# Performance work log

Measured on AMD Instinct MI355X. Metric: run time of the kernel, lower is better.

## Reference

```python
import jax, jax.numpy as jnp
import numpy as np

HEADS = 4
DIM_HEAD = 128

def setup_inputs() -> dict:
    key = jax.random.key(0)
    k1, k2, k3, k4 = jax.random.split(key, 4)
    scale = DIM_HEAD ** -0.5
    return {
        "fmap": jax.random.normal(k1, (16, 512, 32, 32), dtype=jnp.float32),
        "w_qkv": jax.random.normal(k2, (1536, 512), dtype=jnp.float32) * 0.02,
        "height": jax.random.normal(k3, (32, DIM_HEAD), dtype=jnp.float32) * scale,
        "width": jax.random.normal(k4, (32, DIM_HEAD), dtype=jnp.float32) * scale,
    }

def reference(fmap, w_qkv, height, width):
    b, c, h, w = fmap.shape
    scale = DIM_HEAD ** -0.5
    # 1x1 conv == channel GEMM: (b, 3*heads*dim_head, h, w)
    qkv = jnp.einsum('bchw,oc->bohw', fmap, w_qkv)
    # split into q,k,v and reshape to (b, heads, seq, dim_head)
    qkv = qkv.reshape(b, 3, HEADS, DIM_HEAD, h * w)
    q, k, v = (jnp.transpose(qkv[:, i], (0, 1, 3, 2)) for i in range(3))
    # content logits
    sim = jnp.einsum('bhid,bhjd->bhij', q, k) * scale
    # absolute positional bias: emb[(x,y)] = height[x] + width[y]
    emb = (height[:, None, :] + width[None, :, :]).reshape(h * w, DIM_HEAD)
    sim = sim + jnp.einsum('bhid,jd->bhij', q, emb) * scale
    attn = jax.nn.softmax(sim, axis=-1)
    out = jnp.einsum('bhij,bhjd->bhid', attn, v)  # (b, heads, seq, d)
    out = jnp.transpose(out, (0, 1, 3, 2)).reshape(b, HEADS * DIM_HEAD, h, w)
    return out
```

## Files before the change

kernel.cpp:

```cpp
#include <hip/hip_runtime.h>
#include <math.h>

#define HEADS 4
#define DIMH  128
#define NB    16
#define CIN   512
#define SEQ   1024
#define OTOT  1536
#define KQ    (CIN / 8)

typedef __attribute__((ext_vector_type(8)))  short bf16x8;
typedef __attribute__((ext_vector_type(4)))  short bf16x4;
typedef __attribute__((ext_vector_type(4)))  float f32x4;
typedef __attribute__((ext_vector_type(16))) float f32x16;

#define MFMA16(a,b,c) __builtin_amdgcn_mfma_f32_16x16x32_bf16(a,b,c,0,0,0)
#define MFMA32(a,b,c) __builtin_amdgcn_mfma_f32_32x32x16_bf16(a,b,c,0,0,0)

__device__ __forceinline__ short f2bf(float f) {
    unsigned u = __builtin_bit_cast(unsigned, f);
    u = (u + 0x7FFFu + ((u >> 16) & 1u)) >> 16;
    return (short)u;
}
__device__ __forceinline__ unsigned pk2(float lo, float hi) {
    return __builtin_amdgcn_perm(__builtin_bit_cast(unsigned, hi),
                                 __builtin_bit_cast(unsigned, lo), 0x07060302u);
}
union PF8 { unsigned u[4]; bf16x8 v; };

__global__ __launch_bounds__(256) void convert_all(const float* __restrict__ F,
                                                   const float* __restrict__ W,
                                                   short* __restrict__ FT2,
                                                   short* __restrict__ Wb2) {
    const int kq = blockIdx.y;
    if (blockIdx.z == NB) {
        const int o = blockIdx.x * 256 + threadIdx.x;
        float4 v0 = *(const float4*)&W[(size_t)o * CIN + kq * 8];
        float4 v1 = *(const float4*)&W[(size_t)o * CIN + kq * 8 + 4];
        bf16x8 pk = { f2bf(v0.x), f2bf(v0.y), f2bf(v0.z), f2bf(v0.w),
                      f2bf(v1.x), f2bf(v1.y), f2bf(v1.z), f2bf(v1.w) };
        *(bf16x8*)&Wb2[((size_t)kq * OTOT + o) * 8] = pk;
        return;
    }
    if (blockIdx.x >= 4) return;
    const int s = blockIdx.x * 256 + threadIdx.x;
    const int b = blockIdx.z;
    const float* src = F + ((size_t)b * CIN + kq * 8) * SEQ + s;
    float v[8];
    #pragma unroll
    for (int i = 0; i < 8; ++i) v[i] = src[(size_t)i * SEQ];
    bf16x8 pk = { f2bf(v[0]), f2bf(v[1]), f2bf(v[2]), f2bf(v[3]),
                  f2bf(v[4]), f2bf(v[5]), f2bf(v[6]), f2bf(v[7]) };
    *(bf16x8*)&FT2[(((size_t)b * KQ + kq) * SEQ + s) * 8] = pk;
}

__global__ __launch_bounds__(256, 3) void qkv_gemm(
    const short* __restrict__ Wb2, const short* __restrict__ FT2,
    const float* __restrict__ height, const float* __restrict__ width,
    short* __restrict__ Qo, short* __restrict__ Kfo, short* __restrict__ Vfo)
{
    const int L  = blockIdx.x;
    const int x8 = L & 7, m = L >> 3;
    const int g  = x8 + 8 * (m / 12);
    const int oy = m % 12;
    const int b  = g >> 3, sx = g & 7;
    const int o0 = oy * 128, s0 = sx * 128;

    const int t = threadIdx.x, l = t & 63, w = t >> 6;
    const int quad = l >> 4, ln = l & 15;
    const int wrow = (w >> 1) * 64, wcol = (w & 1) * 64;

    const short* Ap = Wb2 + (((size_t)quad * OTOT) + (o0 + wrow + ln)) * 8;
    const short* Bp = FT2 + ((((size_t)b * KQ + quad) * SEQ) + (s0 + wcol + ln)) * 8;

    f32x4 acc[4][4] = {};
    bf16x8 a0[4], b0[4], a1[4], b1[4];

#define GLOADF(ks, af, bfr) { \
    const short* ga = Ap + (size_t)(ks) * 4 * OTOT * 8; \
    const short* gb = Bp + (size_t)(ks) * 4 * SEQ * 8; \
    _Pragma("unroll") for (int i = 0; i < 4; ++i) af[i]  = *(const bf16x8*)(ga + (size_t)i * 16 * 8); \
    _Pragma("unroll") for (int j = 0; j < 4; ++j) bfr[j] = *(const bf16x8*)(gb + (size_t)j * 16 * 8); }
#define COMP(af, bfr) { \
    _Pragma("unroll") for (int i = 0; i < 4; ++i) \
        _Pragma("unroll") for (int j = 0; j < 4; ++j) \
            acc[i][j] = MFMA16(af[i], bfr[j], acc[i][j]); }

    GLOADF(0, a0, b0);
    GLOADF(1, a1, b1);
    for (int ks = 0; ks < 16; ks += 2) {
        COMP(a0, b0);
        if (ks + 2 < 16) GLOADF(ks + 2, a0, b0);
        COMP(a1, b1);
        if (ks + 3 < 16) GLOADF(ks + 3, a1, b1);
    }

    const int sec = o0 >> 9;
    const int h   = (o0 >> 7) & 3;
    const size_t bh = (size_t)b * HEADS + h;

    if (sec == 0) {
        const float qs = 0.08838834764831845f * 1.4426950408889634f;
        #pragma unroll
        for (int ti = 0; ti < 4; ++ti) {
            int d = wrow + ti * 16 + quad * 4;
            #pragma unroll
            for (int tj = 0; tj < 4; ++tj) {
                int s = s0 + wcol + tj * 16 + ln;
                f32x4 a = acc[ti][tj];
                bf16x4 pk4 = { f2bf(a[0]*qs), f2bf(a[1]*qs), f2bf(a[2]*qs), f2bf(a[3]*qs) };
                *(bf16x4*)&Qo[(bh * SEQ + s) * DIMH + d] = pk4;
            }
        }
    } else if (sec == 1) {
        #pragma unroll
        for (int ti = 0; ti < 4; ++ti) {
            int d = wrow + ti * 16 + quad * 4;
            #pragma unroll
            for (int tj = 0; tj < 4; ++tj) {
                int s = s0 + wcol + tj * 16 + ln;
                float4 hv = *(const float4*)&height[(size_t)(s >> 5) * DIMH + d];
                float4 wv = *(const float4*)&width[(size_t)(s & 31) * DIMH + d];
                f32x4 a = acc[ti][tj];
                bf16x4 pk4 = { f2bf(a[0] + hv.x + wv.x), f2bf(a[1] + hv.y + wv.y),
                               f2bf(a[2] + hv.z + wv.z), f2bf(a[3] + hv.w + wv.w) };
                *(bf16x4*)&Kfo[(((size_t)bh * 16 + (d >> 3)) * SEQ + s) * 8 + (d & 7)] = pk4;
            }
        }
    } else {
        const int slot = ((ln >> 2) & 1) * 8 + (ln & 3) + ((ln >> 3) << 2);
        #pragma unroll
        for (int ti = 0; ti < 4; ++ti) {
            int d = wrow + ti * 16 + quad * 4;
            #pragma unroll
            for (int tj = 0; tj < 4; ++tj) {
                int s = s0 + wcol + tj * 16 + ln;
                size_t vb = (((size_t)bh * 64 + (s >> 4)) * DIMH) * 16 + slot;
                f32x4 a = acc[ti][tj];
                #pragma unroll
                for (int r = 0; r < 4; ++r)
                    Vfo[vb + (size_t)(d + r) * 16] = f2bf(a[r]);
            }
        }
    }
}

#define BQ 128
#define BJ 64
#define KSTR 136

#define ATTN_ITER(ti, DO_QK, DO_PRE, DO_BAR)                                        \
{                                                                                   \
    const int rd = (((ti) + 1) & 1) * (BJ * KSTR);                                  \
    const int wr = ((ti) & 1) * (BJ * KSTR);                                        \
    const short* vp0 = Vlane + (size_t)((ti) * 4) * (DIMH * 16);                    \
    bf16x8 vr[4][4];                                                                \
    _Pragma("unroll") for (int gi = 0; gi < 2; ++gi)                                \
      _Pragma("unroll") for (int dc = 0; dc < 4; ++dc)                              \
        vr[gi][dc] = *(const bf16x8*)(vp0 + (size_t)gi * (DIMH * 16) + dc * 32 * 16);\
    int4 kreg[4];                                                                   \
    if (DO_PRE) {                                                                   \
        _Pragma("unroll") for (int p = 0; p < 4; ++p)                               \
            kreg[p] = *(const int4*)(Kg + ((size_t)(p * 4 + w) * SEQ + ((ti) + 2) * BJ + l) * 8); \
    }                                                                               \
    PF8 pf[4];                                                                      \
    _Pragma("unroll") for (int g = 0; g < 4; ++g) {                                 \
        const f32x16& Sh = (g & 2) ? S1 : S0;                                       \
        const int kk = g & 1;                                                       \
        _Pragma("unroll") for (int mm = 0; mm < 4; ++mm) {                          \
            float ea = __builtin_amdgcn_exp2f(Sh[kk * 8 + 2 * mm]);                 \
            float eb = __builtin_amdgcn_exp2f(Sh[kk * 8 + 2 * mm + 1]);             \
            psum += ea + eb;                                                        \
            pf[g].u[mm] = pk2(ea, eb);                                              \
        }                                                                           \
    }                                                                               \
    _Pragma("unroll") for (int gi = 2; gi < 4; ++gi)                                \
      _Pragma("unroll") for (int dc = 0; dc < 4; ++dc)                              \
        vr[gi][dc] = *(const bf16x8*)(vp0 + (size_t)gi * (DIMH * 16) + dc * 32 * 16);\
    if (DO_QK) {                                                                    \
        S0 = (f32x16){}; S1 = (f32x16){};                                           \
        _Pragma("unroll") for (int kc = 0; kc < 8; ++kc) {                          \
            bf16x8 k0 = *(const bf16x8*)&Ks[rd + c31 * KSTR + kc * 16 + h * 8];     \
            bf16x8 k1 = *(const bf16x8*)&Ks[rd + (32 + c31) * KSTR + kc * 16 + h * 8]; \
            S0 = MFMA32(k0, qf[kc], S0);                                            \
            S1 = MFMA32(k1, qf[kc], S1);                                            \
        }                                                                           \
    }                                                                               \
    _Pragma("unroll") for (int g = 0; g < 4; ++g)                                   \
        _Pragma("unroll") for (int dc = 0; dc < 4; ++dc)                            \
            O[dc] = MFMA32(vr[g][dc], pf[g].v, O[dc]);                              \
    if (DO_PRE) {                                                                   \
        _Pragma("unroll") for (int p = 0; p < 4; ++p)                               \
            *(int4*)&Ks[wr + l * KSTR + (p * 4 + w) * 8] = kreg[p];                 \
    }                                                                               \
    if (DO_BAR) __syncthreads();                                                    \
}

__global__ __launch_bounds__(256, 2) void attn(
    const short* __restrict__ Q, const short* __restrict__ Kf,
    const short* __restrict__ Vf, float* __restrict__ out)
{
    __shared__ short Ks[2 * BJ * KSTR];

    const int t = threadIdx.x, l = t & 63, w = t >> 6;
    const int h = l >> 5, c31 = l & 31;

    const int L = blockIdx.x;
    const int x = L & 7, inner = L >> 3;
    const int bh = x * 8 + (inner >> 3);
    const int q0 = (inner & 7) * BQ;
    const size_t obase = (size_t)bh * DIMH * SEQ;

    bf16x8 qf[8];
    {
        const short* Qp = Q + ((size_t)bh * SEQ + (q0 + w * 32 + c31)) * DIMH + h * 8;
        #pragma unroll
        for (int kc = 0; kc < 8; ++kc)
            qf[kc] = *(const bf16x8*)(Qp + kc * 16);
    }

    const short* Kg = Kf + (size_t)bh * 16 * SEQ * 8;
    const short* Vlane = Vf + (size_t)bh * 64 * (DIMH * 16) + (c31 * 16 + h * 8);

    f32x16 O[4] = {};
    float psum = 0.f;

    {
        int4 k0[4], k1[4];
        #pragma unroll
        for (int p = 0; p < 4; ++p) {
            k0[p] = *(const int4*)(Kg + ((size_t)(p * 4 + w) * SEQ + l) * 8);
            k1[p] = *(const int4*)(Kg + ((size_t)(p * 4 + w) * SEQ + BJ + l) * 8);
        }
        #pragma unroll
        for (int p = 0; p < 4; ++p) {
            *(int4*)&Ks[l * KSTR + (p * 4 + w) * 8] = k0[p];
            *(int4*)&Ks[BJ * KSTR + l * KSTR + (p * 4 + w) * 8] = k1[p];
        }
    }
    __syncthreads();

    f32x16 S0 = {}, S1 = {};
    #pragma unroll
    for (int kc = 0; kc < 8; ++kc) {
        bf16x8 k0 = *(const bf16x8*)&Ks[c31 * KSTR + kc * 16 + h * 8];
        bf16x8 k1 = *(const bf16x8*)&Ks[(32 + c31) * KSTR + kc * 16 + h * 8];
        S0 = MFMA32(k0, qf[kc], S0);
        S1 = MFMA32(k1, qf[kc], S1);
    }
    __syncthreads();

    for (int p = 0; p < 7; ++p) {
        const int t0 = 2 * p;
        ATTN_ITER(t0,     true, true, true);
        ATTN_ITER(t0 + 1, true, true, true);
    }
    ATTN_ITER(14, true,  false, false);
    ATTN_ITER(15, false, false, false);

    psum += __shfl_xor(psum, 32);
    float linv = 1.0f / psum;

    #pragma unroll
    for (int dc = 0; dc < 4; ++dc)
        #pragma unroll
        for (int r = 0; r < 16; ++r) {
            int d = dc * 32 + (r & 3) + 8 * (r >> 2) + 4 * h;
            out[obase + (size_t)d * SEQ + q0 + w * 32 + c31] = O[dc][r] * linv;
        }
}

extern "C" void kernel_launch(void* const* d_in, const int* in_sizes, int n_in,
                              void* d_out, int out_size, void* d_ws, size_t ws_size,
                              hipStream_t stream) {
    const float* fmap   = (const float*)d_in[0];
    const float* w_qkv  = (const float*)d_in[1];
    const float* height = (const float*)d_in[2];
    const float* width  = (const float*)d_in[3];
    float* outp = (float*)d_out;

    const size_t n_ft  = (size_t)NB * SEQ * CIN;
    const size_t n_w   = (size_t)OTOT * CIN;
    const size_t n_qkv = (size_t)NB * HEADS * SEQ * DIMH;

    short* FT2 = (short*)d_ws;
    short* Wb2 = FT2 + n_ft;
    short* Qb  = Wb2 + n_w;
    short* Kfb = Qb + n_qkv;
    short* Vfb = Kfb + n_qkv;

    convert_all<<<dim3(6, KQ, NB + 1), 256, 0, stream>>>(fmap, w_qkv, FT2, Wb2);
    qkv_gemm<<<dim3(8 * 12 * NB), 256, 0, stream>>>(
        Wb2, FT2, height, width, Qb, Kfb, Vfb);
    attn<<<dim3(NB * HEADS * (SEQ / BQ)), 256, 0, stream>>>(Qb, Kfb, Vfb, outp);
}
```

Measured before the change: 173.0 us.

## Load K fragments directly from global memory and drop LDS staging and barriers

```diff
diff --git a/kernel.cpp b/kernel.cpp
--- a/kernel.cpp
+++ b/kernel.cpp
@@ -147,22 +147,22 @@
 
 #define BQ 128
 #define BJ 64
-#define KSTR 136
-
-#define ATTN_ITER(ti, DO_QK, DO_PRE, DO_BAR)                                        \
+
+#define ATTN_ITER(ti, DO_QK)                                                        \
 {                                                                                   \
-    const int rd = (((ti) + 1) & 1) * (BJ * KSTR);                                  \
-    const int wr = ((ti) & 1) * (BJ * KSTR);                                        \
+    bf16x8 kn0[8], kn1[8];                                                          \
+    if (DO_QK) {                                                                    \
+        const short* kp = Kg + ((size_t)h * SEQ + ((ti) + 1) * BJ + c31) * 8;       \
+        _Pragma("unroll") for (int kc = 0; kc < 8; ++kc) {                          \
+            kn0[kc] = *(const bf16x8*)(kp + (size_t)(kc * 2) * SEQ * 8);            \
+            kn1[kc] = *(const bf16x8*)(kp + ((size_t)(kc * 2) * SEQ + 32) * 8);     \
+        }                                                                           \
+    }                                                                               \
     const short* vp0 = Vlane + (size_t)((ti) * 4) * (DIMH * 16);                    \
     bf16x8 vr[4][4];                                                                \
     _Pragma("unroll") for (int gi = 0; gi < 2; ++gi)                                \
       _Pragma("unroll") for (int dc = 0; dc < 4; ++dc)                              \
         vr[gi][dc] = *(const bf16x8*)(vp0 + (size_t)gi * (DIMH * 16) + dc * 32 * 16);\
-    int4 kreg[4];                                                                   \
-    if (DO_PRE) {                                                                   \
-        _Pragma("unroll") for (int p = 0; p < 4; ++p)                               \
-            kreg[p] = *(const int4*)(Kg + ((size_t)(p * 4 + w) * SEQ + ((ti) + 2) * BJ + l) * 8); \
-    }                                                                               \
     PF8 pf[4];                                                                      \
     _Pragma("unroll") for (int g = 0; g < 4; ++g) {                                 \
         const f32x16& Sh = (g & 2) ? S1 : S0;                                       \
@@ -174,34 +174,29 @@
             pf[g].u[mm] = pk2(ea, eb);                                              \
         }                                                                           \
     }                                                                               \
+    if (DO_QK) {                                                                    \
+        S0 = (f32x16){}; S1 = (f32x16){};                                           \
+        __builtin_amdgcn_s_setprio(1);                                              \
+        _Pragma("unroll") for (int kc = 0; kc < 8; ++kc) {                          \
+            S0 = MFMA32(kn0[kc], qf[kc], S0);                                       \
+            S1 = MFMA32(kn1[kc], qf[kc], S1);                                       \
+        }                                                                           \
+        __builtin_amdgcn_s_setprio(0);                                              \
+    }                                                                               \
     _Pragma("unroll") for (int gi = 2; gi < 4; ++gi)                                \
       _Pragma("unroll") for (int dc = 0; dc < 4; ++dc)                              \
         vr[gi][dc] = *(const bf16x8*)(vp0 + (size_t)gi * (DIMH * 16) + dc * 32 * 16);\
-    if (DO_QK) {                                                                    \
-        S0 = (f32x16){}; S1 = (f32x16){};                                           \
-        _Pragma("unroll") for (int kc = 0; kc < 8; ++kc) {                          \
-            bf16x8 k0 = *(const bf16x8*)&Ks[rd + c31 * KSTR + kc * 16 + h * 8];     \
-            bf16x8 k1 = *(const bf16x8*)&Ks[rd + (32 + c31) * KSTR + kc * 16 + h * 8]; \
-            S0 = MFMA32(k0, qf[kc], S0);                                            \
-            S1 = MFMA32(k1, qf[kc], S1);                                            \
-        }                                                                           \
-    }                                                                               \
+    __builtin_amdgcn_s_setprio(1);                                                  \
     _Pragma("unroll") for (int g = 0; g < 4; ++g)                                   \
         _Pragma("unroll") for (int dc = 0; dc < 4; ++dc)                            \
             O[dc] = MFMA32(vr[g][dc], pf[g].v, O[dc]);                              \
-    if (DO_PRE) {                                                                   \
-        _Pragma("unroll") for (int p = 0; p < 4; ++p)                               \
-            *(int4*)&Ks[wr + l * KSTR + (p * 4 + w) * 8] = kreg[p];                 \
-    }                                                                               \
-    if (DO_BAR) __syncthreads();                                                    \
+    __builtin_amdgcn_s_setprio(0);                                                  \
 }
 
 __global__ __launch_bounds__(256, 2) void attn(
     const short* __restrict__ Q, const short* __restrict__ Kf,
     const short* __restrict__ Vf, float* __restrict__ out)
 {
-    __shared__ short Ks[2 * BJ * KSTR];
-
     const int t = threadIdx.x, l = t & 63, w = t >> 6;
     const int h = l >> 5, c31 = l & 31;
 
@@ -225,38 +220,22 @@
     f32x16 O[4] = {};
     float psum = 0.f;
 
+    f32x16 S0 = {}, S1 = {};
     {
-        int4 k0[4], k1[4];
-        #pragma unroll
-        for (int p = 0; p < 4; ++p) {
-            k0[p] = *(const int4*)(Kg + ((size_t)(p * 4 + w) * SEQ + l) * 8);
-            k1[p] = *(const int4*)(Kg + ((size_t)(p * 4 + w) * SEQ + BJ + l) * 8);
-        }
-        #pragma unroll
-        for (int p = 0; p < 4; ++p) {
-            *(int4*)&Ks[l * KSTR + (p * 4 + w) * 8] = k0[p];
-            *(int4*)&Ks[BJ * KSTR + l * KSTR + (p * 4 + w) * 8] = k1[p];
-        }
-    }
-    __syncthreads();
-
-    f32x16 S0 = {}, S1 = {};
-    #pragma unroll
-    for (int kc = 0; kc < 8; ++kc) {
-        bf16x8 k0 = *(const bf16x8*)&Ks[c31 * KSTR + kc * 16 + h * 8];
-        bf16x8 k1 = *(const bf16x8*)&Ks[(32 + c31) * KSTR + kc * 16 + h * 8];
-        S0 = MFMA32(k0, qf[kc], S0);
-        S1 = MFMA32(k1, qf[kc], S1);
-    }
-    __syncthreads();
-
-    for (int p = 0; p < 7; ++p) {
-        const int t0 = 2 * p;
-        ATTN_ITER(t0,     true, true, true);
-        ATTN_ITER(t0 + 1, true, true, true);
-    }
-    ATTN_ITER(14, true,  false, false);
-    ATTN_ITER(15, false, false, false);
+        const short* kp = Kg + ((size_t)h * SEQ + c31) * 8;
+        #pragma unroll
+        for (int kc = 0; kc < 8; ++kc) {
+            bf16x8 k0 = *(const bf16x8*)(kp + (size_t)(kc * 2) * SEQ * 8);
+            bf16x8 k1 = *(const bf16x8*)(kp + ((size_t)(kc * 2) * SEQ + 32) * 8);
+            S0 = MFMA32(k0, qf[kc], S0);
+            S1 = MFMA32(k1, qf[kc], S1);
+        }
+    }
+
+    for (int ti = 0; ti < 15; ++ti) {
+        ATTN_ITER(ti, true);
+    }
+    ATTN_ITER(15, false);
 
     psum += __shfl_xor(psum, 32);
     float linv = 1.0f / psum;
```

Result: no change. 175.6 us (+1.5%).

## Stage QKV GEMM operands through LDS with global_load_lds double buffering

Applied to the files above, without the earlier changes.

```diff
diff --git a/kernel.cpp b/kernel.cpp
--- a/kernel.cpp
+++ b/kernel.cpp
@@ -27,6 +27,13 @@
                                  __builtin_bit_cast(unsigned, lo), 0x07060302u);
 }
 union PF8 { unsigned u[4]; bf16x8 v; };
+
+__device__ __forceinline__ void gll16(const short* g, short* l) {
+    __builtin_amdgcn_global_load_lds(
+        (const __attribute__((address_space(1))) unsigned*)g,
+        (__attribute__((address_space(3))) unsigned*)l,
+        16, 0, 0);
+}
 
 __global__ __launch_bounds__(256) void convert_all(const float* __restrict__ F,
                                                    const float* __restrict__ W,
@@ -59,6 +66,9 @@
     const float* __restrict__ height, const float* __restrict__ width,
     short* __restrict__ Qo, short* __restrict__ Kfo, short* __restrict__ Vfo)
 {
+    __shared__ short As[2][4 * 128 * 8];
+    __shared__ short Bs[2][4 * 128 * 8];
+
     const int L  = blockIdx.x;
     const int x8 = L & 7, m = L >> 3;
     const int g  = x8 + 8 * (m / 12);
@@ -70,29 +80,42 @@
     const int quad = l >> 4, ln = l & 15;
     const int wrow = (w >> 1) * 64, wcol = (w & 1) * 64;
 
-    const short* Ap = Wb2 + (((size_t)quad * OTOT) + (o0 + wrow + ln)) * 8;
-    const short* Bp = FT2 + ((((size_t)b * KQ + quad) * SEQ) + (s0 + wcol + ln)) * 8;
+#define STAGE(ks, buf) { \
+    _Pragma("unroll") for (int r = 0; r < 4; ++r) { \
+        const int task = r * 4 + w; \
+        const int p = task >> 1, hf = task & 1; \
+        if (p < 4) { \
+            const short* gsrc = Wb2 + (((size_t)((ks) * 4 + p) * OTOT) + o0 + hf * 64 + l) * 8; \
+            gll16(gsrc, &As[buf][(p * 128 + hf * 64) * 8]); \
+        } else { \
+            const short* gsrc = FT2 + ((((size_t)b * KQ + (ks) * 4 + (p - 4)) * SEQ) + s0 + hf * 64 + l) * 8; \
+            gll16(gsrc, &Bs[buf][((p - 4) * 128 + hf * 64) * 8]); \
+        } \
+    } }
 
     f32x4 acc[4][4] = {};
-    bf16x8 a0[4], b0[4], a1[4], b1[4];
-
-#define GLOADF(ks, af, bfr) { \
-    const short* ga = Ap + (size_t)(ks) * 4 * OTOT * 8; \
-    const short* gb = Bp + (size_t)(ks) * 4 * SEQ * 8; \
-    _Pragma("unroll") for (int i = 0; i < 4; ++i) af[i]  = *(const bf16x8*)(ga + (size_t)i * 16 * 8); \
-    _Pragma("unroll") for (int j = 0; j < 4; ++j) bfr[j] = *(const bf16x8*)(gb + (size_t)j * 16 * 8); }
-#define COMP(af, bfr) { \
-    _Pragma("unroll") for (int i = 0; i < 4; ++i) \
-        _Pragma("unroll") for (int j = 0; j < 4; ++j) \
-            acc[i][j] = MFMA16(af[i], bfr[j], acc[i][j]); }
-
-    GLOADF(0, a0, b0);
-    GLOADF(1, a1, b1);
-    for (int ks = 0; ks < 16; ks += 2) {
-        COMP(a0, b0);
-        if (ks + 2 < 16) GLOADF(ks + 2, a0, b0);
-        COMP(a1, b1);
-        if (ks + 3 < 16) GLOADF(ks + 3, a1, b1);
+
+    STAGE(0, 0);
+    __syncthreads();
+
+    for (int ks = 0; ks < 16; ++ks) {
+        const int cb = ks & 1;
+        if (ks < 15) STAGE(ks + 1, cb ^ 1);
+        const short* Ab = &As[cb][0];
+        const short* Bb = &Bs[cb][0];
+        bf16x8 af[4], bfr[4];
+        #pragma unroll
+        for (int i = 0; i < 4; ++i)
+            af[i]  = *(const bf16x8*)&Ab[((size_t)quad * 128 + wrow + i * 16 + ln) * 8];
+        #pragma unroll
+        for (int j = 0; j < 4; ++j)
+            bfr[j] = *(const bf16x8*)&Bb[((size_t)quad * 128 + wcol + j * 16 + ln) * 8];
+        #pragma unroll
+        for (int i = 0; i < 4; ++i)
+            #pragma unroll
+            for (int j = 0; j < 4; ++j)
+                acc[i][j] = MFMA16(af[i], bfr[j], acc[i][j]);
+        __syncthreads();
     }
 
     const int sec = o0 >> 9;
```

Result: no change. 171.4 us (-1.0%).
